# Kernel tuning notes

Measured on AMD Instinct MI355X. Metric: run time of the kernel, lower is better.

The kernel has to match this reference:

```python
import jax, jax.numpy as jnp
import numpy as np

EPS = 1e-6

def _rms_norm(x):
    xf = x.astype(jnp.float32)
    var = jnp.mean(xf * xf, axis=-1, keepdims=True)
    return (xf * jax.lax.rsqrt(var + EPS)).astype(x.dtype)

def setup_inputs() -> dict:
    key = jax.random.key(0)
    k1, k2 = jax.random.split(key)
    B, N, T, D = 16, 768, 48, 2048
    patches = jax.random.normal(k1, (B, N, D), dtype=jnp.float32)
    task_tokens = jax.random.normal(k2, (B, T, D), dtype=jnp.float32)
    task_token_mask = jnp.ones((B, T), dtype=bool)  # True = valid token
    return {"patches": patches, "task_tokens": task_tokens, "task_token_mask": task_token_mask}

def reference(patches, task_tokens, task_token_mask):
    D = patches.shape[-1]
    scale = 1.0 / np.sqrt(D)
    patches_n = _rms_norm(patches)          # [B,N,D]
    task_n = _rms_norm(task_tokens)         # [B,T,D]
    # additive attention bias: 0 for valid task tokens, finfo.min for masked
    neg = jnp.finfo(patches_n.dtype).min
    bias = jnp.where(task_token_mask[:, None, :], 0.0, neg).astype(patches_n.dtype)  # [B,1,T]
    # scaled dot-product attention: patches attend to task tokens
    logits = jnp.einsum('bnd,btd->bnt', patches_n, task_n) * scale + bias
    attn = jax.nn.softmax(logits, axis=-1)
    queries_raw = jnp.einsum('bnt,btd->bnd', attn, task_n)  # [B,N,D]
    queries = _rms_norm(queries_raw)
    # importance score: each query scores every patch
    score = jnp.einsum('bnd,bmd->bnm', queries, patches_n) * scale  # [B,N,N]
    # differentiable selection (select_soft, noise_scale=None):
    # straight-through: hard one-hot of argmax + soft softmax - stop_grad(soft)
    soft = jax.nn.softmax(score, axis=-1)
    hard = jax.nn.one_hot(jnp.argmax(score, axis=-1), score.shape[-1], dtype=score.dtype)
    sel = hard + soft - jax.lax.stop_gradient(soft)
    return sel
```

## Files before the change

### kernel.cpp

```cpp
#include <hip/hip_runtime.h>
#include <math.h>

#define NB 16
#define NN 768
#define NT 48
#define ND 2048
#define NROW (NB*NN)
#define SCALE 0.02209708691207961f
#define NEGBIG (-3.4028234663852886e38f)
#define TAU 2e-3f
#define KS 512
#define MSPLIT 16
#define MCH (NN/MSPLIT)

typedef _Float16 f16;
typedef f16  f16x8 __attribute__((ext_vector_type(8)));
typedef f16  f16x4 __attribute__((ext_vector_type(4)));
typedef float f32x4 __attribute__((ext_vector_type(4)));

__device__ __forceinline__ void stage16(const void* g, void* l) {
    __builtin_amdgcn_global_load_lds(
        (const __attribute__((address_space(1))) unsigned int*)g,
        (__attribute__((address_space(3))) unsigned int*)l, 16, 0, 0);
}

__device__ __forceinline__ void ins4(float v[4], int idx[4], float nv, int ni) {
    const bool b0 = (v[0] > nv) || (v[0] == nv && idx[0] < ni);
    const bool b1 = (v[1] > nv) || (v[1] == nv && idx[1] < ni);
    const bool b2 = (v[2] > nv) || (v[2] == nv && idx[2] < ni);
    const bool b3 = (v[3] > nv) || (v[3] == nv && idx[3] < ni);
    const int pos = (int)b0 + (int)b1 + (int)b2 + (int)b3;
    if (pos <= 3) { if (pos == 3) { v[3] = nv; idx[3] = ni; } else { v[3] = v[2]; idx[3] = idx[2]; } }
    if (pos <= 2) { if (pos == 2) { v[2] = nv; idx[2] = ni; } else { v[2] = v[1]; idx[2] = idx[1]; } }
    if (pos <= 1) { if (pos == 1) { v[1] = nv; idx[1] = ni; } else { v[1] = v[0]; idx[1] = idx[0]; } }
    if (pos == 0) { v[0] = nv; idx[0] = ni; }
}

__global__ __launch_bounds__(256) void k_prep_task(const float* __restrict__ task,
                                                   float* __restrict__ task_n,
                                                   f16* __restrict__ t_hi,
                                                   f16* __restrict__ t_lo) {
    __shared__ float sred[8];
    const int row = blockIdx.x;
    const float4* src = (const float4*)(task + (size_t)row * ND);
    const int tid = threadIdx.x;
    float4 v0 = src[tid];
    float4 v1 = src[tid + 256];
    float s = v0.x*v0.x + v0.y*v0.y + v0.z*v0.z + v0.w*v0.w
            + v1.x*v1.x + v1.y*v1.y + v1.z*v1.z + v1.w*v1.w;
    #pragma unroll
    for (int off = 32; off > 0; off >>= 1) s += __shfl_down(s, off, 64);
    if ((tid & 63) == 0) sred[tid >> 6] = s;
    __syncthreads();
    if (tid == 0)
        sred[4] = 1.0f / sqrtf((sred[0]+sred[1]+sred[2]+sred[3]) * (1.0f/ND) + 1e-6f);
    __syncthreads();
    const float inv = sred[4];
    const size_t o = (size_t)row * ND;
    f16x4 h0, l0, h1, l1;
    float4 n0, n1;
    #pragma unroll
    for (int e = 0; e < 4; e++) {
        float f0 = (&v0.x)[e] * inv, f1 = (&v1.x)[e] * inv;
        (&n0.x)[e] = f0; (&n1.x)[e] = f1;
        f16 a = (f16)f0; h0[e] = a; l0[e] = (f16)(f0 - (float)a);
        f16 c = (f16)f1; h1[e] = c; l1[e] = (f16)(f1 - (float)c);
    }
    *(float4*)&task_n[o + tid*4]          = n0;
    *(float4*)&task_n[o + (tid+256)*4]    = n1;
    *(f16x4*)&t_hi[o + tid*4]             = h0;
    *(f16x4*)&t_lo[o + tid*4]             = l0;
    *(f16x4*)&t_hi[o + (tid+256)*4]       = h1;
    *(f16x4*)&t_lo[o + (tid+256)*4]       = l1;
}

__global__ __launch_bounds__(256) void k_R(const float* __restrict__ patches,
                                           const f16* __restrict__ t_hi,
                                           const f16* __restrict__ t_lo,
                                           float* __restrict__ Rpart,
                                           float* __restrict__ ssqpart) {
    __shared__ __align__(16) char Ah[64*128], Al[64*128];
    __shared__ __align__(16) char Bh[48*128], Bl[48*128];
    const int rt = blockIdx.x, ks = blockIdx.y, b = blockIdx.z;
    const int tid = threadIdx.x, wid = tid >> 6, lane = tid & 63;
    const int q15 = lane & 15, g4 = lane >> 4;
    const int trow = tid >> 2, tq = tid & 3;
    const int lr = lane >> 3, lgch = (lane & 7) ^ lr;
    const int cxor = q15 & 7;

    const float* gP = patches + ((size_t)(b*NN + rt*64))*ND + ks*KS;
    const f16* gTh = t_hi + (size_t)b*NT*ND + ks*KS;
    const f16* gTl = t_lo + (size_t)b*NT*ND + ks*KS;

    f32x4 acc[3];
    #pragma unroll
    for (int j = 0; j < 3; j++) acc[j] = (f32x4){0.f,0.f,0.f,0.f};
    float ssq = 0.f;

    const float* aptr = gP + (size_t)trow*ND + tq*16;
    float4 v[4], vn[4];
    #pragma unroll
    for (int k = 0; k < 4; k++) v[k] = *(const float4*)(aptr + k*4);

    for (int kk = 0; kk < KS; kk += 64) {
        #pragma unroll
        for (int t2 = 0; t2 < 2; t2++) {
            const int u = wid + 4*t2;
            if (u < 6) {
                stage16(gTh + (size_t)(u*8 + lr)*ND + kk + lgch*8, Bh + u*1024);
                stage16(gTl + (size_t)(u*8 + lr)*ND + kk + lgch*8, Bl + u*1024);
            }
        }
        float lssq = 0.f;
        f16x8 hi8[2], lo8[2];
        #pragma unroll
        for (int k = 0; k < 4; k++)
            #pragma unroll
            for (int e = 0; e < 4; e++) {
                const float f = (&v[k].x)[e];
                lssq += f*f;
                const f16 h = (f16)f;
                hi8[k>>1][(k&1)*4 + e] = h;
                lo8[k>>1][(k&1)*4 + e] = (f16)(f - (float)h);
            }
        lssq += __shfl_xor(lssq, 1, 64);
        lssq += __shfl_xor(lssq, 2, 64);
        if (tq == 0) ssq += lssq;
        const int rb = trow * 128;
        #pragma unroll
        for (int c = 0; c < 2; c++) {
            const int ch = (2*tq + c) ^ (trow & 7);
            *(f16x8*)(Ah + rb + ch*16) = hi8[c];
            *(f16x8*)(Al + rb + ch*16) = lo8[c];
        }
        __syncthreads();
        if (kk + 64 < KS) {
            #pragma unroll
            for (int k = 0; k < 4; k++)
                vn[k] = *(const float4*)(aptr + kk + 64 + k*4);
        }
        #pragma unroll
        for (int ksub = 0; ksub < 2; ksub++) {
            const int chb = ((ksub*4 + g4) ^ cxor) << 4;
            const f16x8 a_h = *(const f16x8*)(Ah + (wid*16 + q15)*128 + chb);
            const f16x8 a_l = *(const f16x8*)(Al + (wid*16 + q15)*128 + chb);
            #pragma unroll
            for (int j = 0; j < 3; j++) {
                const f16x8 b_h = *(const f16x8*)(Bh + (j*16 + q15)*128 + chb);
                const f16x8 b_l = *(const f16x8*)(Bl + (j*16 + q15)*128 + chb);
                acc[j] = __builtin_amdgcn_mfma_f32_16x16x32_f16(a_h, b_h, acc[j], 0, 0, 0);
                acc[j] = __builtin_amdgcn_mfma_f32_16x16x32_f16(a_l, b_h, acc[j], 0, 0, 0);
                acc[j] = __builtin_amdgcn_mfma_f32_16x16x32_f16(a_h, b_l, acc[j], 0, 0, 0);
            }
        }
        __builtin_amdgcn_s_barrier();
        __builtin_amdgcn_sched_barrier(0);
        #pragma unroll
        for (int k = 0; k < 4; k++) v[k] = vn[k];
    }
    const int grow = b*NN + rt*64;
    #pragma unroll
    for (int j = 0; j < 3; j++)
        #pragma unroll
        for (int r = 0; r < 4; r++)
            Rpart[((size_t)ks*NROW + grow + wid*16 + g4*4 + r)*48 + j*16 + q15] = acc[j][r];
    if (tq == 0)
        ssqpart[(size_t)ks*NROW + grow + trow] = ssq;
}

__global__ __launch_bounds__(256) void k_combine(const float* __restrict__ Rpart,
                                                 const float* __restrict__ ssqpart,
                                                 const int* __restrict__ mask,
                                                 float* __restrict__ R,
                                                 float* __restrict__ w,
                                                 float* __restrict__ pinv) {
    const int r = blockIdx.x * 256 + threadIdx.x;
    const int b = r / NN;
    float ss = 0.f;
    #pragma unroll
    for (int ks = 0; ks < 4; ks++) ss += ssqpart[(size_t)ks*NROW + r];
    const float pv = 1.0f / sqrtf(ss * (1.0f/ND) + 1e-6f);
    pinv[r] = pv;
    float l[48];
    float mx = -INFINITY;
    #pragma unroll
    for (int t4 = 0; t4 < 12; t4++) {
        float4 a = {0.f,0.f,0.f,0.f};
        #pragma unroll
        for (int ks = 0; ks < 4; ks++) {
            const float4 p = *(const float4*)&Rpart[((size_t)ks*NROW + r)*48 + t4*4];
            a.x += p.x; a.y += p.y; a.z += p.z; a.w += p.w;
        }
        *(float4*)&R[(size_t)r*48 + t4*4] = a;
        #pragma unroll
        for (int e = 0; e < 4; e++) {
            const int t = t4*4 + e;
            const float bias = mask[b*NT + t] ? 0.0f : NEGBIG;
            l[t] = (&a.x)[e] * pv * SCALE + bias;
            mx = fmaxf(mx, l[t]);
        }
    }
    float sum = 0.f;
    #pragma unroll
    for (int t = 0; t < 48; t++) { l[t] = expf(l[t] - mx); sum += l[t]; }
    const float inv = 1.0f / sum;
    #pragma unroll
    for (int t4 = 0; t4 < 12; t4++) {
        float4 o;
        #pragma unroll
        for (int e = 0; e < 4; e++) (&o.x)[e] = l[t4*4 + e] * inv;
        *(float4*)&w[(size_t)r*48 + t4*4] = o;
    }
}

__global__ __launch_bounds__(256) void k_scoreW(const float* __restrict__ w,
                                                const float* __restrict__ R,
                                                const float* __restrict__ pinv,
                                                float4* __restrict__ part) {
    __shared__ float Rl[MCH*48];
    __shared__ float pl[MCH];
    const int rt = blockIdx.x, ms = blockIdx.y;
    const int tid = threadIdx.x;
    const int row = rt*256 + tid;
    const int b = row / NN;
    const int m0g = b*NN + ms*MCH;
    for (int u = tid; u < MCH*12; u += 256) {
        const int m = u / 12, t4 = u % 12;
        *(float4*)&Rl[m*48 + t4*4] = *(const float4*)&R[((size_t)(m0g + m))*48 + t4*4];
    }
    if (tid < MCH) pl[tid] = pinv[m0g + tid];
    __syncthreads();
    float4 wr[12];
    #pragma unroll
    for (int t4 = 0; t4 < 12; t4++)
        wr[t4] = *(const float4*)&w[(size_t)row*48 + t4*4];
    float tv[4] = {-INFINITY, -INFINITY, -INFINITY, -INFINITY};
    int   ti[4] = {0x7FFFFFFF, 0x7FFFFFFF, 0x7FFFFFFF, 0x7FFFFFFF};
    #pragma unroll 2
    for (int m = 0; m < MCH; m += 4) {
        float s0 = 0.f, s1 = 0.f, s2 = 0.f, s3 = 0.f;
        #pragma unroll
        for (int t4 = 0; t4 < 12; t4++) {
            const float4 r0 = *(const float4*)&Rl[(m+0)*48 + t4*4];
            const float4 r1 = *(const float4*)&Rl[(m+1)*48 + t4*4];
            const float4 r2 = *(const float4*)&Rl[(m+2)*48 + t4*4];
            const float4 r3 = *(const float4*)&Rl[(m+3)*48 + t4*4];
            const float4 wv = wr[t4];
            s0 = fmaf(wv.x, r0.x, s0); s1 = fmaf(wv.x, r1.x, s1);
            s2 = fmaf(wv.x, r2.x, s2); s3 = fmaf(wv.x, r3.x, s3);
            s0 = fmaf(wv.y, r0.y, s0); s1 = fmaf(wv.y, r1.y, s1);
            s2 = fmaf(wv.y, r2.y, s2); s3 = fmaf(wv.y, r3.y, s3);
            s0 = fmaf(wv.z, r0.z, s0); s1 = fmaf(wv.z, r1.z, s1);
            s2 = fmaf(wv.z, r2.z, s2); s3 = fmaf(wv.z, r3.z, s3);
            s0 = fmaf(wv.w, r0.w, s0); s1 = fmaf(wv.w, r1.w, s1);
            s2 = fmaf(wv.w, r2.w, s2); s3 = fmaf(wv.w, r3.w, s3);
        }
        s0 *= pl[m+0]; s1 *= pl[m+1]; s2 *= pl[m+2]; s3 *= pl[m+3];
        const int mg = ms*MCH + m;
        ins4(tv, ti, s0, mg+0);
        ins4(tv, ti, s1, mg+1);
        ins4(tv, ti, s2, mg+2);
        ins4(tv, ti, s3, mg+3);
    }
    part[((size_t)row*MSPLIT + ms)*2]     = make_float4(tv[0], __int_as_float(ti[0]), tv[1], __int_as_float(ti[1]));
    part[((size_t)row*MSPLIT + ms)*2 + 1] = make_float4(tv[2], __int_as_float(ti[2]), tv[3], __int_as_float(ti[3]));
}

__global__ __launch_bounds__(256) void k_final(const float* __restrict__ patches,
                                               const float* __restrict__ task_n,
                                               const float* __restrict__ w,
                                               const float* __restrict__ pinv,
                                               const float4* __restrict__ part,
                                               float* __restrict__ out) {
    __shared__ float qrow[ND];
    __shared__ float wl[48];
    __shared__ int   scand[64];
    __shared__ float swv[4];
    __shared__ int   swi[4];
    __shared__ int   s_idx, s_cnt;
    const int row = blockIdx.x;
    const int b = row / NN;
    const int tid = threadIdx.x, wid = tid >> 6, lane = tid & 63;

    if (wid == 0) {
        const float2 e = ((const float2*)part)[(size_t)row*64 + lane];
        const float myv = e.x;
        const int   myi = __float_as_int(e.y);
        float v = myv; int i = myi;
        #pragma unroll
        for (int off = 1; off <= 32; off <<= 1) {
            const float ov = __shfl_xor(v, off, 64);
            const int   oi = __shfl_xor(i, off, 64);
            if (ov > v || (ov == v && oi < i)) { v = ov; i = oi; }
        }
        const bool in_tau = (myv >= v - TAU);
        const unsigned long long mb  = __ballot(in_tau);
        const unsigned long long mb4 = __ballot(in_tau && ((lane & 3) == 3));
        if (lane == 0) {
            s_idx = i;
            s_cnt = mb4 ? 999 : __popcll(mb);
        }
        if (in_tau) {
            const unsigned long long below = mb & ((lane == 0) ? 0ull : (~0ull >> (64 - lane)));
            scand[__popcll(below)] = myi;
        }
    }
    __syncthreads();
    const int cnt = s_cnt;
    if (cnt > 1) {
        if (tid < 12) *(float4*)&wl[tid*4] = *(const float4*)&w[(size_t)row*48 + tid*4];
        __syncthreads();
        {
            float q[8] = {0.f,0.f,0.f,0.f,0.f,0.f,0.f,0.f};
            for (int t = 0; t < NT; t++) {
                const float wt = wl[t];
                const float* Tn = task_n + ((size_t)(b*NT + t))*ND + tid*8;
                const float4 u0 = *(const float4*)Tn;
                const float4 u1 = *(const float4*)(Tn + 4);
                q[0] = fmaf(wt, u0.x, q[0]); q[1] = fmaf(wt, u0.y, q[1]);
                q[2] = fmaf(wt, u0.z, q[2]); q[3] = fmaf(wt, u0.w, q[3]);
                q[4] = fmaf(wt, u1.x, q[4]); q[5] = fmaf(wt, u1.y, q[5]);
                q[6] = fmaf(wt, u1.z, q[6]); q[7] = fmaf(wt, u1.w, q[7]);
            }
            #pragma unroll
            for (int e2 = 0; e2 < 8; e2++) qrow[tid*8 + e2] = q[e2];
        }
        __syncthreads();
        float bw = -INFINITY; int bi = 0x7FFFFFFF;
        if (cnt != 999) {
            for (int c = wid; c < cnt; c += 4) {
                const int m = scand[c];
                const float* prow = patches + ((size_t)b*NN + m)*ND + lane*32;
                const float* qp = qrow + lane*32;
                float s = 0.f;
                #pragma unroll
                for (int k = 0; k < 8; k++) {
                    const float4 p = *(const float4*)(prow + k*4);
                    const float4 qv = *(const float4*)(qp + k*4);
                    s = fmaf(p.x, qv.x, s); s = fmaf(p.y, qv.y, s);
                    s = fmaf(p.z, qv.z, s); s = fmaf(p.w, qv.w, s);
                }
                #pragma unroll
                for (int off = 32; off > 0; off >>= 1) s += __shfl_down(s, off, 64);
                if (lane == 0) {
                    s *= pinv[b*NN + m];
                    if (s > bw || (s == bw && m < bi)) { bw = s; bi = m; }
                }
            }
        } else {
            for (int m = wid; m < NN; m += 4) {
                const float* prow = patches + ((size_t)b*NN + m)*ND + lane*32;
                const float* qp = qrow + lane*32;
                float s = 0.f;
                #pragma unroll
                for (int k = 0; k < 8; k++) {
                    const float4 p = *(const float4*)(prow + k*4);
                    const float4 qv = *(const float4*)(qp + k*4);
                    s = fmaf(p.x, qv.x, s); s = fmaf(p.y, qv.y, s);
                    s = fmaf(p.z, qv.z, s); s = fmaf(p.w, qv.w, s);
                }
                #pragma unroll
                for (int off = 32; off > 0; off >>= 1) s += __shfl_down(s, off, 64);
                if (lane == 0) {
                    s *= pinv[b*NN + m];
                    if (s > bw || (s == bw && m < bi)) { bw = s; bi = m; }
                }
            }
        }
        if (lane == 0) { swv[wid] = bw; swi[wid] = bi; }
        __syncthreads();
        if (tid == 0) {
            float v = swv[0]; int i = swi[0];
            #pragma unroll
            for (int k = 1; k < 4; k++) {
                if (swv[k] > v || (swv[k] == v && swi[k] < i)) { v = swv[k]; i = swi[k]; }
            }
            s_idx = i;
        }
        __syncthreads();
    }
    const int m = s_idx;
    if (tid < 192) {
        float4 o = {0.f, 0.f, 0.f, 0.f};
        if ((m >> 2) == tid) ((float*)&o)[m & 3] = 1.0f;
        ((float4*)(out + (size_t)row*NN))[tid] = o;
    }
}

extern "C" void kernel_launch(void* const* d_in, const int* in_sizes, int n_in,
                              void* d_out, int out_size, void* d_ws, size_t ws_size,
                              hipStream_t stream) {
    const float* patches = (const float*)d_in[0];
    const float* task    = (const float*)d_in[1];
    const int*   mask    = (const int*)d_in[2];
    float* out = (float*)d_out;

    char* p = (char*)d_ws;
    float* task_n  = (float*)p;  p += (size_t)NB*NT*ND*sizeof(float);
    f16*   t_hi    = (f16*)p;    p += (size_t)NB*NT*ND*sizeof(f16);
    f16*   t_lo    = (f16*)p;    p += (size_t)NB*NT*ND*sizeof(f16);
    float* Rpart   = (float*)p;  p += (size_t)4*NROW*48*sizeof(float);
    float* ssqpart = (float*)p;  p += (size_t)4*NROW*sizeof(float);
    float* R       = (float*)p;  p += (size_t)NROW*48*sizeof(float);
    float* w       = (float*)p;  p += (size_t)NROW*48*sizeof(float);
    float* pinv    = (float*)p;  p += (size_t)NROW*sizeof(float);
    float4* part   = (float4*)p; p += (size_t)NROW*MSPLIT*2*sizeof(float4);

    k_prep_task<<<NB*NT, 256, 0, stream>>>(task, task_n, t_hi, t_lo);
    k_R<<<dim3(NN/64, 4, NB), 256, 0, stream>>>(patches, t_hi, t_lo, Rpart, ssqpart);
    k_combine<<<NROW/256, 256, 0, stream>>>(Rpart, ssqpart, mask, R, w, pinv);
    k_scoreW<<<dim3(NROW/256, MSPLIT), 256, 0, stream>>>(w, R, pinv, part);
    k_final<<<NROW, 256, 0, stream>>>(patches, task_n, w, pinv, part, out);
}
```

Baseline: 116.9 us.

## Manually pipeline patch prefetch with explicit waitcnt and skip top-4 insertion early

The split-K projection loop is unrolled into eight explicit stages that ping-pong two register buffers. The next chunk's global loads are issued before the fp16 hi/lo conversion. The full __syncthreads is replaced with a partial vmcnt wait plus s_barrier, so the prefetch stays in flight while the MFMAs run. Separately, the top-4 score insertion is skipped when the max of four candidates is below the current fourth-best, and the tie-break compare is simplified to rely on ascending index order. This adds fragile hand-written waitcnt counts and sched_barriers that could break if the compiler reorders or counts loads differently.

```diff
diff --git a/kernel.cpp b/kernel.cpp
--- a/kernel.cpp
+++ b/kernel.cpp
@@ -24,11 +24,11 @@
         (__attribute__((address_space(3))) unsigned int*)l, 16, 0, 0);
 }
 
-__device__ __forceinline__ void ins4(float v[4], int idx[4], float nv, int ni) {
-    const bool b0 = (v[0] > nv) || (v[0] == nv && idx[0] < ni);
-    const bool b1 = (v[1] > nv) || (v[1] == nv && idx[1] < ni);
-    const bool b2 = (v[2] > nv) || (v[2] == nv && idx[2] < ni);
-    const bool b3 = (v[3] > nv) || (v[3] == nv && idx[3] < ni);
+__device__ __forceinline__ void ins4m(float v[4], int idx[4], float nv, int ni) {
+    const bool b0 = (v[0] >= nv);
+    const bool b1 = (v[1] >= nv);
+    const bool b2 = (v[2] >= nv);
+    const bool b3 = (v[3] >= nv);
     const int pos = (int)b0 + (int)b1 + (int)b2 + (int)b3;
     if (pos <= 3) { if (pos == 3) { v[3] = nv; idx[3] = ni; } else { v[3] = v[2]; idx[3] = idx[2]; } }
     if (pos <= 2) { if (pos == 2) { v[2] = nv; idx[2] = ni; } else { v[2] = v[1]; idx[2] = idx[1]; } }
@@ -98,11 +98,11 @@
     float ssq = 0.f;
 
     const float* aptr = gP + (size_t)trow*ND + tq*16;
-    float4 v[4], vn[4];
-    #pragma unroll
-    for (int k = 0; k < 4; k++) v[k] = *(const float4*)(aptr + k*4);
-
-    for (int kk = 0; kk < KS; kk += 64) {
+    float4 va[4], vb[4];
+    #pragma unroll
+    for (int k = 0; k < 4; k++) va[k] = *(const float4*)(aptr + k*4);
+
+    auto body = [&](float4 (&v)[4], float4 (&vn)[4], int kk, bool last) {
         #pragma unroll
         for (int t2 = 0; t2 < 2; t2++) {
             const int u = wid + 4*t2;
@@ -111,6 +111,13 @@
                 stage16(gTl + (size_t)(u*8 + lr)*ND + kk + lgch*8, Bl + u*1024);
             }
         }
+        __builtin_amdgcn_sched_barrier(0);
+        if (!last) {
+            #pragma unroll
+            for (int k = 0; k < 4; k++)
+                vn[k] = *(const float4*)(aptr + kk + 64 + k*4);
+        }
+        __builtin_amdgcn_sched_barrier(0);
         float lssq = 0.f;
         f16x8 hi8[2], lo8[2];
         #pragma unroll
@@ -133,12 +140,12 @@
             *(f16x8*)(Ah + rb + ch*16) = hi8[c];
             *(f16x8*)(Al + rb + ch*16) = lo8[c];
         }
-        __syncthreads();
-        if (kk + 64 < KS) {
-            #pragma unroll
-            for (int k = 0; k < 4; k++)
-                vn[k] = *(const float4*)(aptr + kk + 64 + k*4);
-        }
+        __builtin_amdgcn_sched_barrier(0);
+        if (last) asm volatile("s_waitcnt vmcnt(0)" ::: "memory");
+        else      asm volatile("s_waitcnt vmcnt(4)" ::: "memory");
+        asm volatile("s_waitcnt lgkmcnt(0)" ::: "memory");
+        __builtin_amdgcn_s_barrier();
+        __builtin_amdgcn_sched_barrier(0);
         #pragma unroll
         for (int ksub = 0; ksub < 2; ksub++) {
             const int chb = ((ksub*4 + g4) ^ cxor) << 4;
@@ -153,11 +160,20 @@
                 acc[j] = __builtin_amdgcn_mfma_f32_16x16x32_f16(a_h, b_l, acc[j], 0, 0, 0);
             }
         }
+        asm volatile("" ::: "memory");
         __builtin_amdgcn_s_barrier();
         __builtin_amdgcn_sched_barrier(0);
-        #pragma unroll
-        for (int k = 0; k < 4; k++) v[k] = vn[k];
-    }
+    };
+
+    body(va, vb,   0, false);
+    body(vb, va,  64, false);
+    body(va, vb, 128, false);
+    body(vb, va, 192, false);
+    body(va, vb, 256, false);
+    body(vb, va, 320, false);
+    body(va, vb, 384, false);
+    body(vb, va, 448, true);
+
     const int grow = b*NN + rt*64;
     #pragma unroll
     for (int j = 0; j < 3; j++)
@@ -256,11 +272,14 @@
             s2 = fmaf(wv.w, r2.w, s2); s3 = fmaf(wv.w, r3.w, s3);
         }
         s0 *= pl[m+0]; s1 *= pl[m+1]; s2 *= pl[m+2]; s3 *= pl[m+3];
-        const int mg = ms*MCH + m;
-        ins4(tv, ti, s0, mg+0);
-        ins4(tv, ti, s1, mg+1);
-        ins4(tv, ti, s2, mg+2);
-        ins4(tv, ti, s3, mg+3);
+        const float gm = fmaxf(fmaxf(s0, s1), fmaxf(s2, s3));
+        if (gm >= tv[3]) {
+            const int mg = ms*MCH + m;
+            ins4m(tv, ti, s0, mg+0);
+            ins4m(tv, ti, s1, mg+1);
+            ins4m(tv, ti, s2, mg+2);
+            ins4m(tv, ti, s3, mg+3);
+        }
     }
     part[((size_t)row*MSPLIT + ms)*2]     = make_float4(tv[0], __int_as_float(ti[0]), tv[1], __int_as_float(ti[1]));
     part[((size_t)row*MSPLIT + ms)*2 + 1] = make_float4(tv[2], __int_as_float(ti[2]), tv[3], __int_as_float(ti[3]));
```

After: 98.57 us (median of 2 runs). 15.7% less time.
